# Optimization experiments

Measured on AMD Instinct MI355X. Metric: run time of the kernel, lower is better.

The kernel has to match this reference:

```python
import jax, jax.numpy as jnp
import numpy as np

B, T, HID = 1, 1024, 2048
H, DK, DV, M, KW = 16, 128, 128, 128, 4  # heads, key dim, value dim, slots, conv kernel
SCALE = DK ** -0.5
EPS = 1e-5


def short_conv(x, w):
    # causal depthwise conv1d + silu; x: [B,T,C], w: [C,K]
    K = w.shape[1]
    xp = jnp.pad(x, ((0, 0), (K - 1, 0), (0, 0)))
    t = x.shape[1]
    y = sum(xp[:, i:i + t] * w[:, i] for i in range(K))
    return jax.nn.silu(y)


def l2norm(x):
    return x * jax.lax.rsqrt(jnp.sum(x * x, axis=-1, keepdims=True) + 1e-6)


def gsa2_scan(q, k, v, w, g, beta):
    # q,k: [B,T,H,DK]  v: [B,T,H,DV]  w,g: [B,T,H,M]  beta: [B,T,H]
    b = q.shape[0]
    tm = lambda x: jnp.moveaxis(x, 1, 0)  # time-major
    Sk0 = jnp.zeros((b, H, DK, M), q.dtype)  # key->slot memory
    Sv0 = jnp.zeros((b, H, M, DV), q.dtype)  # slot->value memory

    def step(carry, xs):
        Sk, Sv = carry
        q_t, k_t, v_t, w_t, g_t, b_t = xs
        gt = jnp.exp(g_t)  # [B,H,M] gate in (0,1) since g = logsigmoid(.)
        bw = b_t[:, :, None] * w_t  # beta-scaled slot write address [B,H,M]
        Sk = Sk * gt[:, :, None, :] + k_t[..., :, None] * bw[:, :, None, :]
        Sv = Sv * gt[..., None] + bw[..., None] * v_t[:, :, None, :]
        s = jnp.einsum('bhd,bhdm->bhm', q_t, Sk) * SCALE
        a = jax.nn.softmax(s, axis=-1)
        o_t = jnp.einsum('bhm,bhmd->bhd', a, Sv)
        return (Sk, Sv), o_t

    (_, _), o = jax.lax.scan(step, (Sk0, Sv0),
                             (tm(q), tm(k), tm(v), tm(w), tm(g), tm(beta)))
    return jnp.moveaxis(o, 0, 1)  # [B,T,H,DV]


def reference(hidden_states, Wq, Wk, Wv, Ww, cq, ck, cv,
              Wf1, Wf2, Wb, Wg1, Wg2, bg2, norm_w, Wo):
    h = hidden_states  # [B,T,HID]
    q = short_conv(h @ Wq, cq)
    k = short_conv(h @ Wk, ck)
    v = short_conv(h @ Wv, cv)
    w = short_conv(h @ Ww, cv)  # source applies v_conv1d to w (faithful)
    g = jax.nn.log_sigmoid((h @ Wf1) @ Wf2)   # [B,T,H*M]
    beta = jax.nn.sigmoid(h @ Wb)             # [B,T,H]
    rs = lambda x, d: x.reshape(x.shape[0], x.shape[1], -1, d)
    q, k = rs(q, DK), rs(k, DK)
    v = rs(v, DV)
    w = l2norm(rs(w, M))
    g = rs(g, M)
    o = gsa2_scan(q, k, v, w, g, beta)        # [B,T,H,DV]
    gate = rs((h @ Wg1) @ Wg2 + bg2, DV)
    # FusedRMSNormGated with sigmoid activation
    o = o * jax.lax.rsqrt(jnp.mean(o * o, axis=-1, keepdims=True) + EPS)
    o = o * norm_w * jax.nn.sigmoid(gate)
    o = o.reshape(o.shape[0], o.shape[1], -1)
    return o @ Wo


def setup_inputs() -> dict:
    key = jax.random.key(0)
    ks = jax.random.split(key, 16)
    s = 0.02
    return {
        'hidden_states': jax.random.normal(ks[0], (B, T, HID), jnp.float32),
        'Wq': jax.random.normal(ks[1], (HID, H * DK), jnp.float32) * s,
        'Wk': jax.random.normal(ks[2], (HID, H * DK), jnp.float32) * s,
        'Wv': jax.random.normal(ks[3], (HID, H * DV), jnp.float32) * s,
        'Ww': jax.random.normal(ks[4], (HID, H * M), jnp.float32) * s,
        'cq': jax.random.normal(ks[5], (H * DK, KW), jnp.float32) * 0.2,
        'ck': jax.random.normal(ks[6], (H * DK, KW), jnp.float32) * 0.2,
        'cv': jax.random.normal(ks[7], (H * DV, KW), jnp.float32) * 0.2,
        'Wf1': jax.random.normal(ks[8], (HID, DV), jnp.float32) * s,
        'Wf2': jax.random.normal(ks[9], (DV, H * M), jnp.float32) * s,
        'Wb': jax.random.normal(ks[10], (HID, H), jnp.float32) * s,
        'Wg1': jax.random.normal(ks[11], (HID, DV), jnp.float32) * s,
        'Wg2': jax.random.normal(ks[12], (DV, H * DV), jnp.float32) * s,
        'bg2': jnp.zeros((H * DV,), jnp.float32),
        'norm_w': jnp.ones((DV,), jnp.float32),
        'Wo': jax.random.normal(ks[13], (H * DV, HID), jnp.float32) * s,
    }
```

## Files before the change

### kernel.cpp

```cpp
#include <hip/hip_runtime.h>
#include <hip/hip_bf16.h>
#include <stdint.h>

typedef unsigned short u16;
typedef __attribute__((ext_vector_type(8))) short bf16x8;
typedef __attribute__((ext_vector_type(4))) short bf16x4;
typedef __attribute__((ext_vector_type(4))) float f32x4;

#define DEV static __device__ __forceinline__

DEV u16 f2bf(float f){
  union { float f; unsigned u; } x; x.f = f;
  unsigned r = x.u + 0x7fffu + ((x.u >> 16) & 1u);
  return (u16)(r >> 16);
}

DEV float bf2f(u16 u){
  union { unsigned u; float f; } x; x.u = ((unsigned)u) << 16; return x.f;
}

DEV bf16x8 ldfrag(const u16* p){
  bf16x4 a = *(const bf16x4*)p;
  bf16x4 b = *(const bf16x4*)(p+4);
  bf16x8 r;
  r[0]=a[0]; r[1]=a[1]; r[2]=a[2]; r[3]=a[3];
  r[4]=b[0]; r[5]=b[1]; r[6]=b[2]; r[7]=b[3];
  return r;
}

DEV bf16x4 cvt4(float a, float b, float c, float d){
  bf16x4 r; r[0]=(short)f2bf(a); r[1]=(short)f2bf(b); r[2]=(short)f2bf(c); r[3]=(short)f2bf(d);
  return r;
}

DEV void g2l16(const void* g, void* l){
  __builtin_amdgcn_global_load_lds((const __attribute__((address_space(1))) unsigned int*)g,
                                   (__attribute__((address_space(3))) unsigned int*)l,
                                   16, 0, 0);
}

__global__ __launch_bounds__(256)
void transp64_k(const float* __restrict__ Wq, const float* __restrict__ Wk,
                const float* __restrict__ Wv, const float* __restrict__ Ww,
                const float* __restrict__ Wo, u16* __restrict__ WcatT, u16* __restrict__ WoT,
                const float* __restrict__ hX, u16* __restrict__ h_bf,
                const float* __restrict__ Wf1, const float* __restrict__ Wg1,
                const float* __restrict__ Wf2, const float* __restrict__ Wg2,
                u16* __restrict__ WfgT, u16* __restrict__ Wf2T, u16* __restrict__ Wg2T){
  __shared__ float tile[64*65];
  const int z = blockIdx.z;
  if (z == 5){
    int idx = ((blockIdx.y*32 + blockIdx.x)*256 + threadIdx.x)*8;
    float4 v0 = *(const float4*)&hX[idx];
    float4 v1 = *(const float4*)&hX[idx+4];
    ushort4 o0, o1;
    o0.x=f2bf(v0.x); o0.y=f2bf(v0.y); o0.z=f2bf(v0.z); o0.w=f2bf(v0.w);
    o1.x=f2bf(v1.x); o1.y=f2bf(v1.y); o1.z=f2bf(v1.z); o1.w=f2bf(v1.w);
    *(ushort4*)&h_bf[idx]   = o0;
    *(ushort4*)&h_bf[idx+4] = o1;
    return;
  }
  if (z >= 6){
    int rem = blockIdx.y*32 + blockIdx.x;
    if (rem >= 256) return;
    const float* src; u16* dst; int R, C, cx, cy;
    if (z==6){      src=Wf1; dst=WfgT;                  R=2048; C=128;  cx=rem&3;  cy=rem>>2; }
    else if (z==7){ src=Wg1; dst=WfgT+(size_t)128*2048; R=2048; C=128;  cx=rem&3;  cy=rem>>2; }
    else if (z==8){ src=Wf2; dst=Wf2T;                  R=128;  C=2048; cx=rem>>2; cy=rem&3; }
    else {          src=Wg2; dst=Wg2T;                  R=128;  C=2048; cx=rem>>2; cy=rem&3; }
    const int c0 = cx*32, r0 = cy*32;
    const int x = threadIdx.x & 31, y0 = threadIdx.x >> 5;
#pragma unroll
    for (int j=0;j<4;j++){
      int r = y0 + j*8;
      tile[r*33 + x] = src[(size_t)(r0+r)*C + c0 + x];
    }
    __syncthreads();
#pragma unroll
    for (int j=0;j<4;j++){
      int cc = y0 + j*8;
      dst[(size_t)(c0+cc)*R + r0 + x] = f2bf(tile[x*33 + cc]);
    }
    return;
  }
  const float* src = (z==0)?Wq:((z==1)?Wk:((z==2)?Wv:((z==3)?Ww:Wo)));
  u16* dst = (z<4) ? (WcatT + (size_t)z*4194304) : WoT;
  const int c0 = blockIdx.x*64, r0 = blockIdx.y*64;
#pragma unroll
  for (int p=0;p<4;p++){
    int i = threadIdx.x + p*256;
    int r = i>>4, c4 = (i&15)<<2;
    *(float4*)&tile[r*65 + c4] = *(const float4*)&src[(size_t)(r0+r)*2048 + c0 + c4];
  }
  __syncthreads();
#pragma unroll
  for (int p=0;p<4;p++){
    int i = threadIdx.x + p*256;
    int cc = i>>4, r4 = (i&15)<<2;
    ushort4 o;
    o.x = f2bf(tile[(r4+0)*65 + cc]); o.y = f2bf(tile[(r4+1)*65 + cc]);
    o.z = f2bf(tile[(r4+2)*65 + cc]); o.w = f2bf(tile[(r4+3)*65 + cc]);
    *(ushort4*)&dst[(size_t)(c0+cc)*2048 + r0 + r4] = o;
  }
}

template<bool OBF>
__global__ __launch_bounds__(256)
void gemm4_k(const u16* __restrict__ A, const u16* __restrict__ B, void* __restrict__ Cp,
             int K, int lda, int ldb, int ldc){
  __shared__ u16 As[2][128*64];
  __shared__ u16 Bs[2][128*64];
  const int m0 = blockIdx.y*128, n0 = blockIdx.x*128;
  const int tid = threadIdx.x;
  const int wave = tid>>6, lane = tid&63, lr = lane&15, kg = lane>>4;
  const int wm = wave>>1, wn = wave&1;
  const f32x4 vz = {0.f,0.f,0.f,0.f};
  f32x4 acc[4][4];
#pragma unroll
  for (int a=0;a<4;a++)
#pragma unroll
    for (int b=0;b<4;b++) acc[a][b]=vz;

#define STAGE4(buf, k0) do { \
    _Pragma("unroll") \
    for (int p=0;p<4;p++){ \
      int chunk = tid + p*256, r_ = chunk>>3, ci = chunk&7; \
      g2l16(A + (size_t)(m0+r_)*lda + (k0) + ((ci^(r_&7))<<3), &As[buf][chunk*8]); \
    } \
    _Pragma("unroll") \
    for (int p=0;p<4;p++){ \
      int chunk = tid + p*256, r_ = chunk>>3, ci = chunk&7; \
      g2l16(B + (size_t)(n0+r_)*ldb + (k0) + ((ci^(r_&7))<<3), &Bs[buf][chunk*8]); \
    } \
  } while(0)

  const int nt = K>>6;
  STAGE4(0, 0);
  STAGE4(1, 64);
  for (int t=0; t<nt; ++t){
    const int buf = t&1;
    if (t < nt-1) asm volatile("s_waitcnt vmcnt(8)" ::: "memory");
    else          asm volatile("s_waitcnt vmcnt(0)" ::: "memory");
    asm volatile("s_barrier" ::: "memory");
#pragma unroll
    for (int ks=0; ks<2; ++ks){
      bf16x8 af[4], bfv[4];
#pragma unroll
      for (int mi=0;mi<4;mi++){
        int r = wm*64+mi*16+lr;
        af[mi] = *(const bf16x8*)&As[buf][r*64 + (((ks*4+kg)^(r&7))<<3)];
      }
#pragma unroll
      for (int ni=0;ni<4;ni++){
        int r = wn*64+ni*16+lr;
        bfv[ni] = *(const bf16x8*)&Bs[buf][r*64 + (((ks*4+kg)^(r&7))<<3)];
      }
      asm volatile("s_waitcnt lgkmcnt(0)" ::: "memory");
      __builtin_amdgcn_sched_barrier(0);
      __builtin_amdgcn_s_setprio(1);
#pragma unroll
      for (int mi=0;mi<4;mi++)
#pragma unroll
        for (int ni=0;ni<4;ni++)
          acc[mi][ni] = __builtin_amdgcn_mfma_f32_16x16x32_bf16(af[mi], bfv[ni], acc[mi][ni], 0, 0, 0);
      __builtin_amdgcn_s_setprio(0);
      __builtin_amdgcn_sched_barrier(0);
      asm volatile("s_barrier" ::: "memory");
    }
    if (t+2 < nt) STAGE4(buf, (t+2)<<6);
  }
#undef STAGE4
#pragma unroll
  for (int mi=0;mi<4;mi++)
#pragma unroll
    for (int ni=0;ni<4;ni++)
#pragma unroll
      for (int vv=0;vv<4;vv++){
        int row = m0 + wm*64 + mi*16 + kg*4 + vv;
        int col = n0 + wn*64 + ni*16 + lr;
        if (OBF) ((u16*)Cp)[(size_t)row*ldc + col] = f2bf(acc[mi][ni][vv]);
        else     ((float*)Cp)[(size_t)row*ldc + col] = acc[mi][ni][vv];
      }
}

__global__ __launch_bounds__(256)
void gemm4sk_k(const u16* __restrict__ A, const u16* __restrict__ B, float* __restrict__ P,
               int Khalf, int lda, int ldb, int ldc){
  __shared__ u16 As[2][128*64];
  __shared__ u16 Bs[2][128*64];
  const int m0 = blockIdx.y*128, n0 = blockIdx.x*128;
  const int kbase = blockIdx.z*Khalf;
  const int tid = threadIdx.x;
  const int wave = tid>>6, lane = tid&63, lr = lane&15, kg = lane>>4;
  const int wm = wave>>1, wn = wave&1;
  const f32x4 vz = {0.f,0.f,0.f,0.f};
  f32x4 acc[4][4];
#pragma unroll
  for (int a=0;a<4;a++)
#pragma unroll
    for (int b=0;b<4;b++) acc[a][b]=vz;

#define STAGE4(buf, k0) do { \
    _Pragma("unroll") \
    for (int p=0;p<4;p++){ \
      int chunk = tid + p*256, r_ = chunk>>3, ci = chunk&7; \
      g2l16(A + (size_t)(m0+r_)*lda + (k0) + ((ci^(r_&7))<<3), &As[buf][chunk*8]); \
    } \
    _Pragma("unroll") \
    for (int p=0;p<4;p++){ \
      int chunk = tid + p*256, r_ = chunk>>3, ci = chunk&7; \
      g2l16(B + (size_t)(n0+r_)*ldb + (k0) + ((ci^(r_&7))<<3), &Bs[buf][chunk*8]); \
    } \
  } while(0)

  const int nt = Khalf>>6;
  STAGE4(0, kbase);
  STAGE4(1, kbase+64);
  for (int t=0; t<nt; ++t){
    const int buf = t&1;
    if (t < nt-1) asm volatile("s_waitcnt vmcnt(8)" ::: "memory");
    else          asm volatile("s_waitcnt vmcnt(0)" ::: "memory");
    asm volatile("s_barrier" ::: "memory");
#pragma unroll
    for (int ks=0; ks<2; ++ks){
      bf16x8 af[4], bfv[4];
#pragma unroll
      for (int mi=0;mi<4;mi++){
        int r = wm*64+mi*16+lr;
        af[mi] = *(const bf16x8*)&As[buf][r*64 + (((ks*4+kg)^(r&7))<<3)];
      }
#pragma unroll
      for (int ni=0;ni<4;ni++){
        int r = wn*64+ni*16+lr;
        bfv[ni] = *(const bf16x8*)&Bs[buf][r*64 + (((ks*4+kg)^(r&7))<<3)];
      }
      asm volatile("s_waitcnt lgkmcnt(0)" ::: "memory");
      __builtin_amdgcn_sched_barrier(0);
      __builtin_amdgcn_s_setprio(1);
#pragma unroll
      for (int mi=0;mi<4;mi++)
#pragma unroll
        for (int ni=0;ni<4;ni++)
          acc[mi][ni] = __builtin_amdgcn_mfma_f32_16x16x32_bf16(af[mi], bfv[ni], acc[mi][ni], 0, 0, 0);
      __builtin_amdgcn_s_setprio(0);
      __builtin_amdgcn_sched_barrier(0);
      asm volatile("s_barrier" ::: "memory");
    }
    if (t+2 < nt) STAGE4(buf, kbase + ((t+2)<<6));
  }
#undef STAGE4
#pragma unroll
  for (int mi=0;mi<4;mi++)
#pragma unroll
    for (int ni=0;ni<4;ni++)
#pragma unroll
      for (int vv=0;vv<4;vv++){
        int row = m0 + wm*64 + mi*16 + kg*4 + vv;
        int col = n0 + wn*64 + ni*16 + lr;
        P[(size_t)blockIdx.z*2097152 + (size_t)row*ldc + col] = acc[mi][ni][vv];
      }
}

__global__ __launch_bounds__(256)
void addout_k(const float* __restrict__ P, float* __restrict__ out){
  int i = (blockIdx.x*256 + threadIdx.x)*4;
  float4 a = *(const float4*)&P[i];
  float4 b = *(const float4*)&P[2097152 + i];
  float4 s = {a.x+b.x, a.y+b.y, a.z+b.z, a.w+b.w};
  *(float4*)&out[i] = s;
}

__global__ __launch_bounds__(256)
void gemmg_k(const u16* __restrict__ f1g1, const u16* __restrict__ Bf, const u16* __restrict__ Bg,
             float* __restrict__ Ccg, u16* __restrict__ Cgate){
  __shared__ u16 As[128*32];
  __shared__ u16 Bs[128*32];
  const int zz = blockIdx.z;
  const u16* A = f1g1 + zz*128;
  const u16* B = zz ? Bg : Bf;
  const int m0 = blockIdx.y*128, n0 = blockIdx.x*128;
  const int tid = threadIdx.x;
  const int lane = tid & 63, wave = tid >> 6;
  const int wr = wave >> 1, wc = wave & 1;
  const int lr = lane & 15, kg = lane >> 4;
  const f32x4 vzero = {0.f,0.f,0.f,0.f};
  f32x4 acc[4][4];
#pragma unroll
  for (int a=0;a<4;a++)
#pragma unroll
    for (int b=0;b<4;b++) acc[a][b] = vzero;
  const int r0 = tid>>2, s0 = tid&3;
  for (int k0=0;k0<128;k0+=32){
    __syncthreads();
    g2l16(A + (size_t)(m0+r0)*256 + k0 + s0*8, (u16*)As + (size_t)tid*8);
    g2l16(B + (size_t)(n0+r0)*128 + k0 + s0*8, (u16*)Bs + (size_t)tid*8);
    g2l16(A + (size_t)(m0+r0+64)*256 + k0 + s0*8, (u16*)As + (size_t)(tid+256)*8);
    g2l16(B + (size_t)(n0+r0+64)*128 + k0 + s0*8, (u16*)Bs + (size_t)(tid+256)*8);
    __syncthreads();
    bf16x8 af[4], bfv[4];
#pragma unroll
    for (int mi=0;mi<4;mi++) af[mi]  = *(const bf16x8*)(As + (wr*64+mi*16+lr)*32 + kg*8);
#pragma unroll
    for (int ni=0;ni<4;ni++) bfv[ni] = *(const bf16x8*)(Bs + (wc*64+ni*16+lr)*32 + kg*8);
#pragma unroll
    for (int mi=0;mi<4;mi++)
#pragma unroll
      for (int ni=0;ni<4;ni++)
        acc[mi][ni] = __builtin_amdgcn_mfma_f32_16x16x32_bf16(af[mi], bfv[ni], acc[mi][ni], 0, 0, 0);
  }
  if (zz == 0){
#pragma unroll
    for (int ni=0;ni<4;ni++){
      float p[4][4]; float s[4];
#pragma unroll
      for (int mi=0;mi<4;mi++){
        float run = 0.f;
#pragma unroll
        for (int vv=0;vv<4;vv++){
          float v = acc[mi][ni][vv];
          v = fminf(v,0.f) - __logf(1.f + __expf(-fabsf(v)));
          run += v; p[mi][vv] = run;
        }
        s[mi] = run;
      }
      float M = 0.f; float base[4];
#pragma unroll
      for (int mi=0;mi<4;mi++){
        float a0 = __shfl(s[mi], lr);
        float a1 = __shfl(s[mi], lr+16);
        float a2 = __shfl(s[mi], lr+32);
        float a3 = __shfl(s[mi], lr+48);
        float before = 0.f;
        if (kg>0) before += a0;
        if (kg>1) before += a1;
        if (kg>2) before += a2;
        base[mi] = M + before;
        M += a0+a1+a2+a3;
      }
#pragma unroll
      for (int mi=0;mi<4;mi++)
#pragma unroll
        for (int vv=0;vv<4;vv++){
          int row = m0 + wr*64 + mi*16 + kg*4 + vv;
          int col = n0 + wc*64 + ni*16 + lr;
          Ccg[(size_t)row*2048 + col] = base[mi] + p[mi][vv];
        }
    }
  } else {
#pragma unroll
    for (int mi=0;mi<4;mi++)
#pragma unroll
      for (int ni=0;ni<4;ni++)
#pragma unroll
        for (int vv=0;vv<4;vv++){
          int row = m0 + wr*64 + mi*16 + kg*4 + vv;
          int col = n0 + wc*64 + ni*16 + lr;
          Cgate[(size_t)row*2048 + col] = f2bf(acc[mi][ni][vv]);
        }
  }
}

__global__ __launch_bounds__(256)
void gemmsk_k(const u16* __restrict__ A, const u16* __restrict__ B, float* __restrict__ P,
              int lda, int ldb){
  __shared__ u16 As[128*32];
  __shared__ u16 Bs[128*32];
  const int m0 = blockIdx.y*128, n0 = blockIdx.x*128;
  const int kbase = blockIdx.z*128;
  const int tid = threadIdx.x;
  const int lane = tid & 63, wave = tid >> 6;
  const int wr = wave >> 1, wc = wave & 1;
  const int lr = lane & 15, kg = lane >> 4;
  const f32x4 vzero = {0.f,0.f,0.f,0.f};
  f32x4 acc[4][4];
#pragma unroll
  for (int a=0;a<4;a++)
#pragma unroll
    for (int b=0;b<4;b++) acc[a][b] = vzero;
  const int r0 = tid>>2, s0 = tid&3;
  for (int k0=kbase;k0<kbase+128;k0+=32){
    __syncthreads();
    g2l16(A + (size_t)(m0+r0)*lda + k0 + s0*8, (u16*)As + (size_t)tid*8);
    g2l16(B + (size_t)(n0+r0)*ldb + k0 + s0*8, (u16*)Bs + (size_t)tid*8);
    g2l16(A + (size_t)(m0+r0+64)*lda + k0 + s0*8, (u16*)As + (size_t)(tid+256)*8);
    g2l16(B + (size_t)(n0+r0+64)*ldb + k0 + s0*8, (u16*)Bs + (size_t)(tid+256)*8);
    __syncthreads();
    bf16x8 af[4], bfv[4];
#pragma unroll
    for (int mi=0;mi<4;mi++) af[mi]  = *(const bf16x8*)(As + (wr*64+mi*16+lr)*32 + kg*8);
#pragma unroll
    for (int ni=0;ni<4;ni++) bfv[ni] = *(const bf16x8*)(Bs + (wc*64+ni*16+lr)*32 + kg*8);
#pragma unroll
    for (int mi=0;mi<4;mi++)
#pragma unroll
      for (int ni=0;ni<4;ni++)
        acc[mi][ni] = __builtin_amdgcn_mfma_f32_16x16x32_bf16(af[mi], bfv[ni], acc[mi][ni], 0, 0, 0);
  }
#pragma unroll
  for (int mi=0;mi<4;mi++)
#pragma unroll
    for (int ni=0;ni<4;ni++)
#pragma unroll
      for (int vv=0;vv<4;vv++){
        int row = m0 + wr*64 + mi*16 + kg*4 + vv;
        int col = n0 + wc*64 + ni*16 + lr;
        P[(size_t)blockIdx.z*262144 + (size_t)row*256 + col] = acc[mi][ni][vv];
      }
}

__global__ __launch_bounds__(256)
void reduce16_k(const float* __restrict__ P, u16* __restrict__ out){
  int i = (blockIdx.x*256 + threadIdx.x)*4;
  float4 s = *(const float4*)&P[i];
#pragma unroll
  for (int z=1;z<16;z++){
    float4 p = *(const float4*)&P[(size_t)z*262144 + i];
    s.x+=p.x; s.y+=p.y; s.z+=p.z; s.w+=p.w;
  }
  ushort4 o; o.x=f2bf(s.x); o.y=f2bf(s.y); o.z=f2bf(s.z); o.w=f2bf(s.w);
  *(ushort4*)&out[i] = o;
}

__global__ __launch_bounds__(256)
void beta_k(const u16* __restrict__ h, const float* __restrict__ Wb, float* __restrict__ betab){
  __shared__ float hrow[2048];
  __shared__ float red[16][5];
  const int t = blockIdx.x, tid = threadIdx.x;
  {
    int b8 = tid*8;
    ushort4 a = *(const ushort4*)&h[(size_t)t*2048 + b8];
    ushort4 b = *(const ushort4*)&h[(size_t)t*2048 + b8 + 4];
    hrow[b8+0]=bf2f(a.x); hrow[b8+1]=bf2f(a.y); hrow[b8+2]=bf2f(a.z); hrow[b8+3]=bf2f(a.w);
    hrow[b8+4]=bf2f(b.x); hrow[b8+5]=bf2f(b.y); hrow[b8+6]=bf2f(b.z); hrow[b8+7]=bf2f(b.w);
  }
  __syncthreads();
  float part[16];
#pragma unroll
  for (int n=0;n<16;n++) part[n]=0.f;
  for (int j=0;j<8;j++){
    int kk = tid + j*256;
    float hv = hrow[kk];
    const float4* wr4 = (const float4*)&Wb[(size_t)kk*16];
    float4 w0=wr4[0], w1=wr4[1], w2=wr4[2], w3=wr4[3];
    part[0]+=hv*w0.x; part[1]+=hv*w0.y; part[2]+=hv*w0.z; part[3]+=hv*w0.w;
    part[4]+=hv*w1.x; part[5]+=hv*w1.y; part[6]+=hv*w1.z; part[7]+=hv*w1.w;
    part[8]+=hv*w2.x; part[9]+=hv*w2.y; part[10]+=hv*w2.z; part[11]+=hv*w2.w;
    part[12]+=hv*w3.x; part[13]+=hv*w3.y; part[14]+=hv*w3.z; part[15]+=hv*w3.w;
  }
#pragma unroll
  for (int n=0;n<16;n++){
    float s = part[n];
#pragma unroll
    for (int off=1;off<64;off<<=1) s += __shfl_xor(s, off);
    if ((tid&63)==0) red[n][tid>>6] = s;
  }
  __syncthreads();
  if (tid < 16){
    float s = red[tid][0]+red[tid][1]+red[tid][2]+red[tid][3];
    betab[t*16+tid] = 1.f/(1.f+__expf(-s));
  }
}

__global__ __launch_bounds__(256)
void conv_k(const u16* __restrict__ raw, const float* __restrict__ cq,
            const float* __restrict__ ck, const float* __restrict__ cv,
            const float* __restrict__ betab,
            u16* __restrict__ qo, u16* __restrict__ ko,
            u16* __restrict__ vo, float* __restrict__ bwout){
  __shared__ float red[2][2][4];
  int idx = blockIdx.x*256 + threadIdx.x;
  int cgl = idx & 8191, tb = idx >> 13;
  int which = cgl >> 11, cc = cgl & 2047;
  const float* wt = (which==0)?cq:((which==1)?ck:cv);
  float4 w4 = *(const float4*)&wt[cc*4];
  int t0 = tb*4;
  float x[7];
#pragma unroll
  for (int j=0;j<7;j++){
    int t = t0 - 3 + j;
    x[j] = (t >= 0) ? bf2f(raw[(size_t)t*8192 + cgl]) : 0.f;
  }
  float y[4];
#pragma unroll
  for (int j=0;j<4;j++){
    float yy = x[j]*w4.x + x[j+1]*w4.y + x[j+2]*w4.z + x[j+3]*w4.w;
    y[j] = yy / (1.f + __expf(-yy));
  }
  if (which < 3){
    u16* outb = (which==0)?qo:((which==1)?ko:vo);
#pragma unroll
    for (int j=0;j<4;j++)
      outb[(size_t)(t0+j)*2048 + cc] = f2bf(y[j]);
  } else {
    const int hh = threadIdx.x >> 7;
    const int wh = (threadIdx.x >> 6) & 1;
    float ss[4];
#pragma unroll
    for (int j=0;j<4;j++){
      float s = y[j]*y[j];
#pragma unroll
      for (int off=1;off<64;off<<=1) s += __shfl_xor(s, off);
      ss[j] = s;
    }
    if ((threadIdx.x & 63) == 0){
#pragma unroll
      for (int j=0;j<4;j++) red[hh][wh][j] = ss[j];
    }
    __syncthreads();
    const int h = cc >> 7;
#pragma unroll
    for (int j=0;j<4;j++){
      float tot = red[hh][0][j] + red[hh][1][j];
      float r = rsqrtf(tot + 1e-6f) * betab[(t0+j)*16 + h];
      bwout[(size_t)(t0+j)*2048 + cc] = y[j]*r;
    }
  }
}

__global__ __launch_bounds__(256)
void phaseA_k(const u16* __restrict__ k, const u16* __restrict__ v,
              const float* __restrict__ bw, const float* __restrict__ cg,
              u16* __restrict__ DSkT, u16* __restrict__ DSvT){
  __shared__ u16 UT[128*68];
  __shared__ u16 KT[128*68];
  __shared__ u16 VT[128*68];
  __shared__ float Gt[128];
  const int bx=blockIdx.x, h=bx&15, c=bx>>4, tid=threadIdx.x;
  const int w=tid>>6, lane=tid&63, lr=lane&15, kg=lane>>4;
  if (tid<128) Gt[tid] = cg[(size_t)(c*64+63)*2048 + h*128 + tid];
  __syncthreads();
#pragma unroll
  for (int j=0;j<8;j++){
    int f4=tid+j*256, r=f4>>5, c4=(f4&31)<<2;
    size_t g=(size_t)(c*64+r)*2048 + h*128 + c4;
    ushort4 kv=*(const ushort4*)&k[g];
    ushort4 vv=*(const ushort4*)&v[g];
    float4 bv=*(const float4*)&bw[g];
    float4 cv=*(const float4*)&cg[g];
    float u0=bv.x*__expf(Gt[c4+0]-cv.x);
    float u1=bv.y*__expf(Gt[c4+1]-cv.y);
    float u2=bv.z*__expf(Gt[c4+2]-cv.z);
    float u3=bv.w*__expf(Gt[c4+3]-cv.w);
    KT[(c4+0)*68+r]=kv.x; KT[(c4+1)*68+r]=kv.y;
    KT[(c4+2)*68+r]=kv.z; KT[(c4+3)*68+r]=kv.w;
    VT[(c4+0)*68+r]=vv.x; VT[(c4+1)*68+r]=vv.y;
    VT[(c4+2)*68+r]=vv.z; VT[(c4+3)*68+r]=vv.w;
    UT[(c4+0)*68+r]=f2bf(u0);   UT[(c4+1)*68+r]=f2bf(u1);
    UT[(c4+2)*68+r]=f2bf(u2);   UT[(c4+3)*68+r]=f2bf(u3);
  }
  __syncthreads();
  const f32x4 vz = {0.f,0.f,0.f,0.f};
  {
    f32x4 acc[2][8];
#pragma unroll
    for (int a=0;a<2;a++)
#pragma unroll
      for (int b=0;b<8;b++) acc[a][b]=vz;
#pragma unroll
    for (int ks=0;ks<2;ks++){
      bf16x8 a0=ldfrag(&UT[(w*32   +lr)*68 + ks*32+kg*8]);
      bf16x8 a1=ldfrag(&UT[(w*32+16+lr)*68 + ks*32+kg*8]);
#pragma unroll
      for (int nj=0;nj<8;nj++){
        bf16x8 b=ldfrag(&KT[(nj*16+lr)*68 + ks*32+kg*8]);
        acc[0][nj]=__builtin_amdgcn_mfma_f32_16x16x32_bf16(a0,b,acc[0][nj],0,0,0);
        acc[1][nj]=__builtin_amdgcn_mfma_f32_16x16x32_bf16(a1,b,acc[1][nj],0,0,0);
      }
    }
#pragma unroll
    for (int mi2=0;mi2<2;mi2++)
#pragma unroll
      for (int nj=0;nj<8;nj++)
#pragma unroll
        for (int vv2=0;vv2<4;vv2++)
          DSkT[(size_t)bx*16384 + (size_t)(w*32+mi2*16+kg*4+vv2)*128 + nj*16+lr] = f2bf(acc[mi2][nj][vv2]);
  }
  {
    f32x4 acc[2][8];
#pragma unroll
    for (int a=0;a<2;a++)
#pragma unroll
      for (int b=0;b<8;b++) acc[a][b]=vz;
#pragma unroll
    for (int ks=0;ks<2;ks++){
      bf16x8 a0=ldfrag(&VT[(w*32   +lr)*68 + ks*32+kg*8]);
      bf16x8 a1=ldfrag(&VT[(w*32+16+lr)*68 + ks*32+kg*8]);
#pragma unroll
      for (int nj=0;nj<8;nj++){
        bf16x8 b=ldfrag(&UT[(nj*16+lr)*68 + ks*32+kg*8]);
        acc[0][nj]=__builtin_amdgcn_mfma_f32_16x16x32_bf16(a0,b,acc[0][nj],0,0,0);
        acc[1][nj]=__builtin_amdgcn_mfma_f32_16x16x32_bf16(a1,b,acc[1][nj],0,0,0);
      }
    }
#pragma unroll
    for (int mi2=0;mi2<2;mi2++)
#pragma unroll
      for (int nj=0;nj<8;nj++)
#pragma unroll
        for (int vv2=0;vv2<4;vv2++)
          DSvT[(size_t)bx*16384 + (size_t)(w*32+mi2*16+kg*4+vv2)*128 + nj*16+lr] = f2bf(acc[mi2][nj][vv2]);
  }
}

__global__ __launch_bounds__(256)
void phaseB_k(const u16* __restrict__ DSk, const u16* __restrict__ DSv,
              const float* __restrict__ cg, u16* __restrict__ Sk0, u16* __restrict__ Sv0){
  unsigned idx = blockIdx.x*256u + threadIdx.x;
  int sel  = idx >> 18;
  int h    = (idx >> 14) & 15;
  int flat = idx & 16383;
  int mdec = sel ? (flat & 127) : (flat >> 7);
  const u16* DS = sel ? DSv : DSk;
  u16* S = sel ? Sv0 : Sk0;
  float cur = 0.f;
  for (int c=0;c<16;c++){
    size_t sb = ((size_t)(c*16+h))*16384 + flat;
    S[sb] = f2bf(cur);
    float gd = __expf(cg[(size_t)(c*64+63)*2048 + h*128 + mdec]);
    cur = cur*gd + bf2f(DS[sb]);
  }
}

__global__ __launch_bounds__(256)
void phaseC_k(const u16* __restrict__ q, const u16* __restrict__ k,
              const u16* __restrict__ v, const float* __restrict__ bw,
              const float* __restrict__ cg, const u16* __restrict__ SkT,
              const u16* __restrict__ SvT, const u16* __restrict__ gate,
              const float* __restrict__ bg2, const float* __restrict__ nw,
              u16* __restrict__ Obf){
  __shared__ u16 Qb[64*132];
  __shared__ u16 KV[8704];
  __shared__ u16 Bws[64*132];
  __shared__ u16 BwT[128*68];
  __shared__ u16 Ssb[64*68];
  __shared__ u16 SkL[128*132];
  __shared__ u16 SvL[128*132];
  __shared__ float cgm[128];
  __shared__ float ecgm[128];
  const int bx=blockIdx.x, h=bx&15, c=bx>>4, tid=threadIdx.x;
  const int w=tid>>6, lane=tid&63, lr=lane&15, kg=lane>>4;
  const float SCALE = 0.088388347648318447f;
  const f32x4 vz = {0.f,0.f,0.f,0.f};
  if (tid<128){ float t=cg[(size_t)(c*64+31)*2048 + h*128 + tid]; cgm[tid]=t; ecgm[tid]=__expf(t); }
  __syncthreads();
#pragma unroll
  for (int j=0;j<8;j++){
    int f4=tid+j*256, r=f4>>5, c4=(f4&31)<<2;
    size_t g=(size_t)(c*64+r)*2048 + h*128 + c4;
    *(ushort4*)&Qb[r*132+c4] = *(const ushort4*)&q[g];
    *(ushort4*)&KV[r*132+c4] = *(const ushort4*)&k[g];
    float4 bv=*(const float4*)&bw[g];
    float4 cv=*(const float4*)&cg[g];
    float b0=bv.x*__expf(cgm[c4+0]-cv.x);
    float b1=bv.y*__expf(cgm[c4+1]-cv.y);
    float b2=bv.z*__expf(cgm[c4+2]-cv.z);
    float b3=bv.w*__expf(cgm[c4+3]-cv.w);
    bf16x4 bb = cvt4(b0,b1,b2,b3);
    *(bf16x4*)&Bws[r*132+c4] = bb;
    BwT[(c4+0)*68+r]=(u16)bb[0]; BwT[(c4+1)*68+r]=(u16)bb[1];
    BwT[(c4+2)*68+r]=(u16)bb[2]; BwT[(c4+3)*68+r]=(u16)bb[3];
  }
  __syncthreads();
  {
    f32x4 acc1[4];
#pragma unroll
    for (int a=0;a<4;a++) acc1[a]=vz;
#pragma unroll
    for (int ks=0;ks<4;ks++){
      bf16x8 aq = ldfrag(&Qb[(w*16+lr)*132 + ks*32+kg*8]);
#pragma unroll
      for (int ni=0;ni<4;ni++){
        bf16x8 bk = ldfrag(&KV[(ni*16+lr)*132 + ks*32+kg*8]);
        acc1[ni]=__builtin_amdgcn_mfma_f32_16x16x32_bf16(aq,bk,acc1[ni],0,0,0);
      }
    }
#pragma unroll
    for (int ni=0;ni<4;ni++)
#pragma unroll
      for (int vv2=0;vv2<4;vv2++){
        int row=w*16+kg*4+vv2, col=ni*16+lr;
        Ssb[row*68+col] = (col<=row) ? f2bf(acc1[ni][vv2]) : (u16)0;
      }
  }
  __syncthreads();
#pragma unroll
  for (int j=0;j<8;j++){
    int f4=tid+j*256, r=f4>>5, c4=(f4&31)<<2;
    ushort4 vv=*(const ushort4*)&v[(size_t)(c*64+r)*2048 + h*128 + c4];
    KV[(c4+0)*68+r]=vv.x; KV[(c4+1)*68+r]=vv.y;
    KV[(c4+2)*68+r]=vv.z; KV[(c4+3)*68+r]=vv.w;
  }
#pragma unroll
  for (int j=0;j<16;j++){
    int f4=tid+j*256, r=f4>>5, c4=(f4&31)<<2;
    ushort4 s4=*(const ushort4*)&SkT[(size_t)bx*16384 + (size_t)r*128 + c4];
    float em=ecgm[r];
    *(bf16x4*)&SkL[r*132+c4]=cvt4(bf2f(s4.x)*em, bf2f(s4.y)*em, bf2f(s4.z)*em, bf2f(s4.w)*em);
  }
#pragma unroll
  for (int j=0;j<16;j++){
    int f4=tid+j*256, r=f4>>5, c4=(f4&31)<<2;
    ushort4 s4=*(const ushort4*)&SvT[(size_t)bx*16384 + (size_t)r*128 + c4];
    *(bf16x4*)&SvL[r*132+c4]=cvt4(bf2f(s4.x)*ecgm[c4+0], bf2f(s4.y)*ecgm[c4+1],
                                  bf2f(s4.z)*ecgm[c4+2], bf2f(s4.w)*ecgm[c4+3]);
  }
  f32x4 zac[8];
#pragma unroll
  for (int a=0;a<8;a++) zac[a]=vz;
#pragma unroll
  for (int ks=0;ks<2;ks++){
    bf16x8 as_ = ldfrag(&Ssb[(w*16+lr)*68 + ks*32+kg*8]);
#pragma unroll
    for (int ni=0;ni<8;ni++){
      bf16x8 bb = ldfrag(&BwT[(ni*16+lr)*68 + ks*32+kg*8]);
      zac[ni]=__builtin_amdgcn_mfma_f32_16x16x32_bf16(as_,bb,zac[ni],0,0,0);
    }
  }
  __syncthreads();
#pragma unroll
  for (int dt=0;dt<4;dt++){
    bf16x8 aq = ldfrag(&Qb[(w*16+lr)*132 + dt*32+kg*8]);
#pragma unroll
    for (int ni=0;ni<8;ni++){
      bf16x8 bs = ldfrag(&SkL[(ni*16+lr)*132 + dt*32+kg*8]);
      zac[ni]=__builtin_amdgcn_mfma_f32_16x16x32_bf16(aq,bs,zac[ni],0,0,0);
    }
  }
  float dec[4][8], zz[4][8];
#pragma unroll
  for (int vv2=0;vv2<4;vv2++)
#pragma unroll
    for (int ni=0;ni<8;ni++) zz[vv2][ni]=zac[ni][vv2];
#pragma unroll
  for (int vv2=0;vv2<4;vv2++){
    size_t gr=(size_t)(c*64+w*16+kg*4+vv2)*2048 + h*128;
#pragma unroll
    for (int ni=0;ni<8;ni++){
      float cgv = cg[gr + ni*16+lr];
      dec[vv2][ni] = __expf(cgv - cgm[ni*16+lr]);
    }
  }
#pragma unroll
  for (int vv2=0;vv2<4;vv2++){
    float mx=-3.0e38f;
#pragma unroll
    for (int ni=0;ni<8;ni++){ zz[vv2][ni] *= SCALE*dec[vv2][ni]; mx=fmaxf(mx,zz[vv2][ni]); }
    mx=fmaxf(mx,__shfl_xor(mx,1)); mx=fmaxf(mx,__shfl_xor(mx,2));
    mx=fmaxf(mx,__shfl_xor(mx,4)); mx=fmaxf(mx,__shfl_xor(mx,8));
    float sum=0.f;
#pragma unroll
    for (int ni=0;ni<8;ni++){ zz[vv2][ni]=__expf(zz[vv2][ni]-mx); sum+=zz[vv2][ni]; }
    sum+=__shfl_xor(sum,1); sum+=__shfl_xor(sum,2);
    sum+=__shfl_xor(sum,4); sum+=__shfl_xor(sum,8);
    float inv=1.f/sum;
#pragma unroll
    for (int ni=0;ni<8;ni++) zz[vv2][ni] *= inv*dec[vv2][ni];
  }
#pragma unroll
  for (int vv2=0;vv2<4;vv2++)
#pragma unroll
    for (int ni=0;ni<8;ni++)
      Qb[(w*16+kg*4+vv2)*132 + ni*16+lr] = f2bf(zz[vv2][ni]);
  {
    f32x4 acc4[4];
#pragma unroll
    for (int a=0;a<4;a++) acc4[a]=vz;
#pragma unroll
    for (int ks=0;ks<4;ks++){
      bf16x8 aa = ldfrag(&Qb[(w*16+lr)*132 + ks*32+kg*8]);
#pragma unroll
      for (int ni=0;ni<4;ni++){
        bf16x8 bb = ldfrag(&Bws[(ni*16+lr)*132 + ks*32+kg*8]);
        acc4[ni]=__builtin_amdgcn_mfma_f32_16x16x32_bf16(aa,bb,acc4[ni],0,0,0);
      }
    }
#pragma unroll
    for (int ni=0;ni<4;ni++)
#pragma unroll
      for (int vv2=0;vv2<4;vv2++){
        int row=w*16+kg*4+vv2, col=ni*16+lr;
        Ssb[row*68+col] = (col<=row) ? f2bf(acc4[ni][vv2]) : (u16)0;
      }
  }
  f32x4 oac[8];
#pragma unroll
  for (int a=0;a<8;a++) oac[a]=vz;
#pragma unroll
  for (int ks=0;ks<2;ks++){
    bf16x8 ap = ldfrag(&Ssb[(w*16+lr)*68 + ks*32+kg*8]);
#pragma unroll
    for (int ni=0;ni<8;ni++){
      bf16x8 bv2 = ldfrag(&KV[(ni*16+lr)*68 + ks*32+kg*8]);
      oac[ni]=__builtin_amdgcn_mfma_f32_16x16x32_bf16(ap,bv2,oac[ni],0,0,0);
    }
  }
#pragma unroll
  for (int mt=0;mt<4;mt++){
    bf16x8 aa = ldfrag(&Qb[(w*16+lr)*132 + mt*32+kg*8]);
#pragma unroll
    for (int ni=0;ni<8;ni++){
      bf16x8 bs = ldfrag(&SvL[(ni*16+lr)*132 + mt*32+kg*8]);
      oac[ni]=__builtin_amdgcn_mfma_f32_16x16x32_bf16(aa,bs,oac[ni],0,0,0);
    }
  }
#pragma unroll
  for (int vv2=0;vv2<4;vv2++){
    float ss = 0.f;
#pragma unroll
    for (int ni=0;ni<8;ni++) ss += oac[ni][vv2]*oac[ni][vv2];
    ss += __shfl_xor(ss,1); ss += __shfl_xor(ss,2);
    ss += __shfl_xor(ss,4); ss += __shfl_xor(ss,8);
    float rr = rsqrtf(ss*(1.f/128.f) + 1e-5f);
    int row = c*64 + w*16 + kg*4 + vv2;
#pragma unroll
    for (int ni=0;ni<8;ni++){
      int colh = ni*16+lr;
      int col  = h*128 + colh;
      float g = bf2f(gate[(size_t)row*2048 + col]) + bg2[col];
      float val = oac[ni][vv2]*rr*nw[colh]*(1.f/(1.f+__expf(-g)));
      Obf[(size_t)row*2048 + col] = f2bf(val);
    }
  }
}

extern "C" void kernel_launch(void* const* d_in, const int* in_sizes, int n_in,
                              void* d_out, int out_size, void* d_ws, size_t ws_size,
                              hipStream_t stream){
  (void)in_sizes; (void)n_in; (void)out_size; (void)ws_size;
  const float* hX   = (const float*)d_in[0];
  const float* Wq   = (const float*)d_in[1];
  const float* Wk   = (const float*)d_in[2];
  const float* Wv   = (const float*)d_in[3];
  const float* Ww   = (const float*)d_in[4];
  const float* cq   = (const float*)d_in[5];
  const float* ck   = (const float*)d_in[6];
  const float* cv   = (const float*)d_in[7];
  const float* Wf1  = (const float*)d_in[8];
  const float* Wf2  = (const float*)d_in[9];
  const float* Wb   = (const float*)d_in[10];
  const float* Wg1  = (const float*)d_in[11];
  const float* Wg2  = (const float*)d_in[12];
  const float* bg2  = (const float*)d_in[13];
  const float* nw   = (const float*)d_in[14];
  const float* Wo   = (const float*)d_in[15];
  char* ws = (char*)d_ws;
  u16*   h_bf  = (u16*)  (ws + 0);
  u16*   WcatT = (u16*)  (ws + 4194304);
  u16*   Sk0   = (u16*)  (ws + 4194304);
  u16*   Sv0   = (u16*)  (ws + 20971520);
  u16*   WoT   = (u16*)  (ws + 37748736);
  u16*   WfgT  = (u16*)  (ws + 46137344);
  u16*   Wf2T  = (u16*)  (ws + 47185920);
  u16*   Wg2T  = (u16*)  (ws + 47710208);
  u16*   qkvw  = (u16*)  (ws + 48234496);
  u16*   DSk   = (u16*)  (ws + 48234496);
  u16*   DSv   = (u16*)  (ws + 56623104);
  float* Pw    = (float*)(ws + 48234496);
  u16*   gateb = (u16*)  (ws + 65011712);
  u16*   qb    = (u16*)  (ws + 81788928);
  u16*   kb    = (u16*)  (ws + 90177536);
  u16*   vb    = (u16*)  (ws + 98566144);
  float* P8    = (float*)(ws + 106954752);
  float* bwb   = (float*)(ws + 115343360);
  u16*   f1g1  = (u16*)  (ws + 123731968);
  float* cgb   = (float*)(ws + 132644864);
  float* betab = (float*)(ws + 141033472);
  u16*   Obf   = (u16*)  (ws + 141099008);
  float* outp  = (float*)d_out;

  transp64_k<<<dim3(32,32,10),256,0,stream>>>(Wq, Wk, Wv, Ww, Wo, WcatT, WoT, hX, h_bf,
                                              Wf1, Wg1, Wf2, Wg2, WfgT, Wf2T, Wg2T);

  gemm4_k<true><<<dim3(64,8),256,0,stream>>>(h_bf, WcatT, qkvw, 2048, 2048, 2048, 8192);
  gemmsk_k<<<dim3(2,8,16),256,0,stream>>>(h_bf, WfgT, P8, 2048, 2048);
  reduce16_k<<<256,256,0,stream>>>(P8, f1g1);
  gemmg_k<<<dim3(16,8,2),256,0,stream>>>(f1g1, Wf2T, Wg2T, cgb, gateb);
  beta_k<<<1024,256,0,stream>>>(h_bf, Wb, betab);

  conv_k<<<8192,256,0,stream>>>(qkvw, cq, ck, cv, betab, qb, kb, vb, bwb);

  phaseA_k<<<256,256,0,stream>>>(kb, vb, bwb, cgb, DSk, DSv);
  phaseB_k<<<2048,256,0,stream>>>(DSk, DSv, cgb, Sk0, Sv0);
  phaseC_k<<<256,256,0,stream>>>(qb, kb, vb, bwb, cgb, Sk0, Sv0, gateb, bg2, nw, Obf);

  gemm4sk_k<<<dim3(16,8,2),256,0,stream>>>(Obf, WoT, Pw, 1024, 2048, 2048, 2048);
  addout_k<<<2048,256,0,stream>>>(Pw, outp);
}
```

Baseline: 180.8 us.

## Fold beta projection into split-K GEMM, store partials in bf16, atomic-add output

The Wb projection becomes extra padded columns of the split-K Wf1/Wg1 GEMM, so the separate beta kernel is gone and the sigmoid is applied inside the reduction kernel. Split-K partials and the bw buffer are now stored in bf16 instead of fp32, roughly halving their traffic. The final output split-K GEMM atomically adds into a zeroed output, replacing the partial-buffer write plus the add kernel. The cost is extra bf16 rounding of the partials and bw, plus atomic contention and a memset.

Result: faster. 176.4 us, median of 2 (-2.5%).

```diff
diff --git a/kernel.cpp b/kernel.cpp
--- a/kernel.cpp
+++ b/kernel.cpp
@@ -46,6 +46,7 @@
                 const float* __restrict__ hX, u16* __restrict__ h_bf,
                 const float* __restrict__ Wf1, const float* __restrict__ Wg1,
                 const float* __restrict__ Wf2, const float* __restrict__ Wg2,
+                const float* __restrict__ Wb,
                 u16* __restrict__ WfgT, u16* __restrict__ Wf2T, u16* __restrict__ Wg2T){
   __shared__ float tile[64*65];
   const int z = blockIdx.z;
@@ -60,6 +61,20 @@
     *(ushort4*)&h_bf[idx+4] = o1;
     return;
   }
+  if (z == 10){
+    int rem = blockIdx.y*32 + blockIdx.x;
+    if (rem >= 256) return;
+    int cx = rem & 63, cy = rem >> 6;
+    const int x = threadIdx.x & 31, y0 = threadIdx.x >> 5;
+    int k = cx*32 + x;
+#pragma unroll
+    for (int j=0;j<4;j++){
+      int rpad = cy*32 + y0 + j*8;
+      float v = (rpad < 16) ? Wb[(size_t)k*16 + rpad] : 0.f;
+      WfgT[(size_t)(256+rpad)*2048 + k] = f2bf(v);
+    }
+    return;
+  }
   if (z >= 6){
     int rem = blockIdx.y*32 + blockIdx.x;
     if (rem >= 256) return;
@@ -184,7 +199,7 @@
 }
 
 __global__ __launch_bounds__(256)
-void gemm4sk_k(const u16* __restrict__ A, const u16* __restrict__ B, float* __restrict__ P,
+void gemm4sk_k(const u16* __restrict__ A, const u16* __restrict__ B, float* __restrict__ out,
                int Khalf, int lda, int ldb, int ldc){
   __shared__ u16 As[2][128*64];
   __shared__ u16 Bs[2][128*64];
@@ -257,17 +272,8 @@
       for (int vv=0;vv<4;vv++){
         int row = m0 + wm*64 + mi*16 + kg*4 + vv;
         int col = n0 + wn*64 + ni*16 + lr;
-        P[(size_t)blockIdx.z*2097152 + (size_t)row*ldc + col] = acc[mi][ni][vv];
-      }
-}
-
-__global__ __launch_bounds__(256)
-void addout_k(const float* __restrict__ P, float* __restrict__ out){
-  int i = (blockIdx.x*256 + threadIdx.x)*4;
-  float4 a = *(const float4*)&P[i];
-  float4 b = *(const float4*)&P[2097152 + i];
-  float4 s = {a.x+b.x, a.y+b.y, a.z+b.z, a.w+b.w};
-  *(float4*)&out[i] = s;
+        unsafeAtomicAdd(&out[(size_t)row*ldc + col], acc[mi][ni][vv]);
+      }
 }
 
 __global__ __launch_bounds__(256)
@@ -292,9 +298,9 @@
   const int r0 = tid>>2, s0 = tid&3;
   for (int k0=0;k0<128;k0+=32){
     __syncthreads();
-    g2l16(A + (size_t)(m0+r0)*256 + k0 + s0*8, (u16*)As + (size_t)tid*8);
+    g2l16(A + (size_t)(m0+r0)*384 + k0 + s0*8, (u16*)As + (size_t)tid*8);
     g2l16(B + (size_t)(n0+r0)*128 + k0 + s0*8, (u16*)Bs + (size_t)tid*8);
-    g2l16(A + (size_t)(m0+r0+64)*256 + k0 + s0*8, (u16*)As + (size_t)(tid+256)*8);
+    g2l16(A + (size_t)(m0+r0+64)*384 + k0 + s0*8, (u16*)As + (size_t)(tid+256)*8);
     g2l16(B + (size_t)(n0+r0+64)*128 + k0 + s0*8, (u16*)Bs + (size_t)(tid+256)*8);
     __syncthreads();
     bf16x8 af[4], bfv[4];
@@ -361,7 +367,7 @@
 }
 
 __global__ __launch_bounds__(256)
-void gemmsk_k(const u16* __restrict__ A, const u16* __restrict__ B, float* __restrict__ P,
+void gemmsk_k(const u16* __restrict__ A, const u16* __restrict__ B, u16* __restrict__ P,
               int lda, int ldb){
   __shared__ u16 As[128*32];
   __shared__ u16 Bs[128*32];
@@ -404,60 +410,29 @@
       for (int vv=0;vv<4;vv++){
         int row = m0 + wr*64 + mi*16 + kg*4 + vv;
         int col = n0 + wc*64 + ni*16 + lr;
-        P[(size_t)blockIdx.z*262144 + (size_t)row*256 + col] = acc[mi][ni][vv];
-      }
-}
-
-__global__ __launch_bounds__(256)
-void reduce16_k(const float* __restrict__ P, u16* __restrict__ out){
-  int i = (blockIdx.x*256 + threadIdx.x)*4;
-  float4 s = *(const float4*)&P[i];
-#pragma unroll
-  for (int z=1;z<16;z++){
-    float4 p = *(const float4*)&P[(size_t)z*262144 + i];
-    s.x+=p.x; s.y+=p.y; s.z+=p.z; s.w+=p.w;
-  }
-  ushort4 o; o.x=f2bf(s.x); o.y=f2bf(s.y); o.z=f2bf(s.z); o.w=f2bf(s.w);
-  *(ushort4*)&out[i] = o;
-}
-
-__global__ __launch_bounds__(256)
-void beta_k(const u16* __restrict__ h, const float* __restrict__ Wb, float* __restrict__ betab){
-  __shared__ float hrow[2048];
-  __shared__ float red[16][5];
-  const int t = blockIdx.x, tid = threadIdx.x;
-  {
-    int b8 = tid*8;
-    ushort4 a = *(const ushort4*)&h[(size_t)t*2048 + b8];
-    ushort4 b = *(const ushort4*)&h[(size_t)t*2048 + b8 + 4];
-    hrow[b8+0]=bf2f(a.x); hrow[b8+1]=bf2f(a.y); hrow[b8+2]=bf2f(a.z); hrow[b8+3]=bf2f(a.w);
-    hrow[b8+4]=bf2f(b.x); hrow[b8+5]=bf2f(b.y); hrow[b8+6]=bf2f(b.z); hrow[b8+7]=bf2f(b.w);
-  }
-  __syncthreads();
-  float part[16];
-#pragma unroll
-  for (int n=0;n<16;n++) part[n]=0.f;
-  for (int j=0;j<8;j++){
-    int kk = tid + j*256;
-    float hv = hrow[kk];
-    const float4* wr4 = (const float4*)&Wb[(size_t)kk*16];
-    float4 w0=wr4[0], w1=wr4[1], w2=wr4[2], w3=wr4[3];
-    part[0]+=hv*w0.x; part[1]+=hv*w0.y; part[2]+=hv*w0.z; part[3]+=hv*w0.w;
-    part[4]+=hv*w1.x; part[5]+=hv*w1.y; part[6]+=hv*w1.z; part[7]+=hv*w1.w;
-    part[8]+=hv*w2.x; part[9]+=hv*w2.y; part[10]+=hv*w2.z; part[11]+=hv*w2.w;
-    part[12]+=hv*w3.x; part[13]+=hv*w3.y; part[14]+=hv*w3.z; part[15]+=hv*w3.w;
-  }
-#pragma unroll
-  for (int n=0;n<16;n++){
-    float s = part[n];
-#pragma unroll
-    for (int off=1;off<64;off<<=1) s += __shfl_xor(s, off);
-    if ((tid&63)==0) red[n][tid>>6] = s;
-  }
-  __syncthreads();
-  if (tid < 16){
-    float s = red[tid][0]+red[tid][1]+red[tid][2]+red[tid][3];
-    betab[t*16+tid] = 1.f/(1.f+__expf(-s));
+        P[(size_t)blockIdx.z*393216 + (size_t)row*384 + col] = f2bf(acc[mi][ni][vv]);
+      }
+}
+
+__global__ __launch_bounds__(256)
+void reduceb_k(const u16* __restrict__ P, u16* __restrict__ out, float* __restrict__ betab){
+  int i4 = (blockIdx.x*256 + threadIdx.x)*4;
+  float s0=0.f, s1=0.f, s2=0.f, s3=0.f;
+#pragma unroll
+  for (int z=0;z<16;z++){
+    ushort4 p = *(const ushort4*)&P[(size_t)z*393216 + i4];
+    s0+=bf2f(p.x); s1+=bf2f(p.y); s2+=bf2f(p.z); s3+=bf2f(p.w);
+  }
+  ushort4 o; o.x=f2bf(s0); o.y=f2bf(s1); o.z=f2bf(s2); o.w=f2bf(s3);
+  *(ushort4*)&out[i4] = o;
+  int col = i4 % 384;
+  if (col >= 256 && col < 272){
+    int row = i4 / 384;
+    float* bp = &betab[row*16 + (col-256)];
+    bp[0] = 1.f/(1.f+__expf(-s0));
+    bp[1] = 1.f/(1.f+__expf(-s1));
+    bp[2] = 1.f/(1.f+__expf(-s2));
+    bp[3] = 1.f/(1.f+__expf(-s3));
   }
 }
 
@@ -466,7 +441,7 @@
             const float* __restrict__ ck, const float* __restrict__ cv,
             const float* __restrict__ betab,
             u16* __restrict__ qo, u16* __restrict__ ko,
-            u16* __restrict__ vo, float* __restrict__ bwout){
+            u16* __restrict__ vo, u16* __restrict__ bwout){
   __shared__ float red[2][2][4];
   int idx = blockIdx.x*256 + threadIdx.x;
   int cgl = idx & 8191, tb = idx >> 13;
@@ -512,14 +487,14 @@
     for (int j=0;j<4;j++){
       float tot = red[hh][0][j] + red[hh][1][j];
       float r = rsqrtf(tot + 1e-6f) * betab[(t0+j)*16 + h];
-      bwout[(size_t)(t0+j)*2048 + cc] = y[j]*r;
+      bwout[(size_t)(t0+j)*2048 + cc] = f2bf(y[j]*r);
     }
   }
 }
 
 __global__ __launch_bounds__(256)
 void phaseA_k(const u16* __restrict__ k, const u16* __restrict__ v,
-              const float* __restrict__ bw, const float* __restrict__ cg,
+              const u16* __restrict__ bw, const float* __restrict__ cg,
               u16* __restrict__ DSkT, u16* __restrict__ DSvT){
   __shared__ u16 UT[128*68];
   __shared__ u16 KT[128*68];
@@ -535,12 +510,12 @@
     size_t g=(size_t)(c*64+r)*2048 + h*128 + c4;
     ushort4 kv=*(const ushort4*)&k[g];
     ushort4 vv=*(const ushort4*)&v[g];
-    float4 bv=*(const float4*)&bw[g];
+    ushort4 bv=*(const ushort4*)&bw[g];
     float4 cv=*(const float4*)&cg[g];
-    float u0=bv.x*__expf(Gt[c4+0]-cv.x);
-    float u1=bv.y*__expf(Gt[c4+1]-cv.y);
-    float u2=bv.z*__expf(Gt[c4+2]-cv.z);
-    float u3=bv.w*__expf(Gt[c4+3]-cv.w);
+    float u0=bf2f(bv.x)*__expf(Gt[c4+0]-cv.x);
+    float u1=bf2f(bv.y)*__expf(Gt[c4+1]-cv.y);
+    float u2=bf2f(bv.z)*__expf(Gt[c4+2]-cv.z);
+    float u3=bf2f(bv.w)*__expf(Gt[c4+3]-cv.w);
     KT[(c4+0)*68+r]=kv.x; KT[(c4+1)*68+r]=kv.y;
     KT[(c4+2)*68+r]=kv.z; KT[(c4+3)*68+r]=kv.w;
     VT[(c4+0)*68+r]=vv.x; VT[(c4+1)*68+r]=vv.y;
@@ -623,7 +598,7 @@
 
 __global__ __launch_bounds__(256)
 void phaseC_k(const u16* __restrict__ q, const u16* __restrict__ k,
-              const u16* __restrict__ v, const float* __restrict__ bw,
+              const u16* __restrict__ v, const u16* __restrict__ bw,
               const float* __restrict__ cg, const u16* __restrict__ SkT,
               const u16* __restrict__ SvT, const u16* __restrict__ gate,
               const float* __restrict__ bg2, const float* __restrict__ nw,
@@ -649,12 +624,12 @@
     size_t g=(size_t)(c*64+r)*2048 + h*128 + c4;
     *(ushort4*)&Qb[r*132+c4] = *(const ushort4*)&q[g];
     *(ushort4*)&KV[r*132+c4] = *(const ushort4*)&k[g];
-    float4 bv=*(const float4*)&bw[g];
+    ushort4 bv=*(const ushort4*)&bw[g];
     float4 cv=*(const float4*)&cg[g];
-    float b0=bv.x*__expf(cgm[c4+0]-cv.x);
-    float b1=bv.y*__expf(cgm[c4+1]-cv.y);
-    float b2=bv.z*__expf(cgm[c4+2]-cv.z);
-    float b3=bv.w*__expf(cgm[c4+3]-cv.w);
+    float b0=bf2f(bv.x)*__expf(cgm[c4+0]-cv.x);
+    float b1=bf2f(bv.y)*__expf(cgm[c4+1]-cv.y);
+    float b2=bf2f(bv.z)*__expf(cgm[c4+2]-cv.z);
+    float b3=bf2f(bv.w)*__expf(cgm[c4+3]-cv.w);
     bf16x4 bb = cvt4(b0,b1,b2,b3);
     *(bf16x4*)&Bws[r*132+c4] = bb;
     BwT[(c4+0)*68+r]=(u16)bb[0]; BwT[(c4+1)*68+r]=(u16)bb[1];
@@ -849,33 +824,31 @@
   u16*   Sk0   = (u16*)  (ws + 4194304);
   u16*   Sv0   = (u16*)  (ws + 20971520);
   u16*   WoT   = (u16*)  (ws + 37748736);
-  u16*   WfgT  = (u16*)  (ws + 46137344);
   u16*   Wf2T  = (u16*)  (ws + 47185920);
   u16*   Wg2T  = (u16*)  (ws + 47710208);
   u16*   qkvw  = (u16*)  (ws + 48234496);
   u16*   DSk   = (u16*)  (ws + 48234496);
   u16*   DSv   = (u16*)  (ws + 56623104);
-  float* Pw    = (float*)(ws + 48234496);
   u16*   gateb = (u16*)  (ws + 65011712);
   u16*   qb    = (u16*)  (ws + 81788928);
   u16*   kb    = (u16*)  (ws + 90177536);
   u16*   vb    = (u16*)  (ws + 98566144);
-  float* P8    = (float*)(ws + 106954752);
-  float* bwb   = (float*)(ws + 115343360);
+  u16*   P8    = (u16*)  (ws + 106954752);
+  u16*   bwb   = (u16*)  (ws + 119537664);
   u16*   f1g1  = (u16*)  (ws + 123731968);
+  u16*   WfgT  = (u16*)  (ws + 124518400);
   float* cgb   = (float*)(ws + 132644864);
   float* betab = (float*)(ws + 141033472);
   u16*   Obf   = (u16*)  (ws + 141099008);
   float* outp  = (float*)d_out;
 
-  transp64_k<<<dim3(32,32,10),256,0,stream>>>(Wq, Wk, Wv, Ww, Wo, WcatT, WoT, hX, h_bf,
-                                              Wf1, Wg1, Wf2, Wg2, WfgT, Wf2T, Wg2T);
+  transp64_k<<<dim3(32,32,11),256,0,stream>>>(Wq, Wk, Wv, Ww, Wo, WcatT, WoT, hX, h_bf,
+                                              Wf1, Wg1, Wf2, Wg2, Wb, WfgT, Wf2T, Wg2T);
 
   gemm4_k<true><<<dim3(64,8),256,0,stream>>>(h_bf, WcatT, qkvw, 2048, 2048, 2048, 8192);
-  gemmsk_k<<<dim3(2,8,16),256,0,stream>>>(h_bf, WfgT, P8, 2048, 2048);
-  reduce16_k<<<256,256,0,stream>>>(P8, f1g1);
+  gemmsk_k<<<dim3(3,8,16),256,0,stream>>>(h_bf, WfgT, P8, 2048, 2048);
+  reduceb_k<<<384,256,0,stream>>>(P8, f1g1, betab);
   gemmg_k<<<dim3(16,8,2),256,0,stream>>>(f1g1, Wf2T, Wg2T, cgb, gateb);
-  beta_k<<<1024,256,0,stream>>>(h_bf, Wb, betab);
 
   conv_k<<<8192,256,0,stream>>>(qkvw, cq, ck, cv, betab, qb, kb, vb, bwb);
 
@@ -883,6 +856,6 @@
   phaseB_k<<<2048,256,0,stream>>>(DSk, DSv, cgb, Sk0, Sv0);
   phaseC_k<<<256,256,0,stream>>>(qb, kb, vb, bwb, cgb, Sk0, Sv0, gateb, bg2, nw, Obf);
 
-  gemm4sk_k<<<dim3(16,8,2),256,0,stream>>>(Obf, WoT, Pw, 1024, 2048, 2048, 2048);
-  addout_k<<<2048,256,0,stream>>>(Pw, outp);
-}
+  hipMemsetAsync(outp, 0, (size_t)1024*2048*4, stream);
+  gemm4sk_k<<<dim3(16,8,2),256,0,stream>>>(Obf, WoT, outp, 1024, 2048, 2048, 2048);
+}
```
